# Performance work log

Hardware: AMD Instinct MI355X
Metric: run time of the kernel (lower is better)

The kernel has to match this reference:

```python
import jax, jax.numpy as jnp
import numpy as np
from jax import lax

B, C, HW = 8, 512, 32
NH = 8            # num_heads
NG = 32           # num_groups
HD = C // NH      # head_size = 64
EPS = 1e-6


def group_norm(x, gamma, beta, groups=NG, eps=EPS):
    b, c, h, w = x.shape
    xr = x.reshape(b, groups, c // groups, h, w)
    mu = xr.mean(axis=(2, 3, 4), keepdims=True)
    var = xr.var(axis=(2, 3, 4), keepdims=True)
    xn = ((xr - mu) / jnp.sqrt(var + eps)).reshape(b, c, h, w)
    return xn * gamma[None, :, None, None] + beta[None, :, None, None]


def conv2d(x, w, b):
    y = lax.conv_general_dilated(x, w, (1, 1), 'SAME',
                                 dimension_numbers=('NCHW', 'OIHW', 'NCHW'))
    return y + b[None, :, None, None]


def setup_inputs() -> dict:
    key = jax.random.key(0)
    ks = jax.random.split(key, 24)
    f32 = jnp.float32

    def lin(k, out_d, in_d):
        return (jax.random.normal(k, (out_d, in_d), f32) / np.sqrt(in_d)).astype(f32)

    inp = {
        'hidden_states': jax.random.normal(ks[0], (B, C, HW, HW), f32),
        'pre_g': jnp.ones(C, f32), 'pre_b': jnp.zeros(C, f32),
        'norm_g': jnp.ones(C, f32), 'norm_b': jnp.zeros(C, f32),
        'post_g': jnp.ones(C, f32), 'post_b': jnp.zeros(C, f32),
        'pos_emb': jax.random.normal(ks[1], (1, C, 32, 32), f32) * 0.02,
        'sa_w1': (jax.random.normal(ks[2], (C // 8, C, 1, 1), f32) / np.sqrt(C)),
        'sa_b1': jnp.zeros(C // 8, f32),
        'sa_w2': (jax.random.normal(ks[3], (C // 8, C // 8, 3, 3), f32) / np.sqrt(9 * C // 8)),
        'sa_b2': jnp.zeros(C // 8, f32),
        'sa_w3': (jax.random.normal(ks[4], (1, C // 8, 1, 1), f32) / np.sqrt(C // 8)),
        'sa_b3': jnp.zeros(1, f32),
        'wq': lin(ks[5], C, C), 'wk': lin(ks[6], C, C), 'wv': lin(ks[7], C, C),
        'wq0': lin(ks[8], C // 2, C), 'wk0': lin(ks[9], C // 2, C), 'wv0': lin(ks[10], C // 2, C),
        'wq1': lin(ks[11], C // 2, C), 'wk1': lin(ks[12], C // 2, C), 'wv1': lin(ks[13], C // 2, C),
        'ff_w1': lin(ks[14], C, 2 * C), 'ff_b1': jnp.zeros(C, f32),
        'ff_w2': lin(ks[15], C, C), 'ff_b2': jnp.zeros(C, f32),
        'out_w': lin(ks[16], C, C), 'out_b': jnp.zeros(C, f32),
    }
    return inp


def reference(hidden_states, pre_g, pre_b, norm_g, norm_b, post_g, post_b,
              pos_emb, sa_w1, sa_b1, sa_w2, sa_b2, sa_w3, sa_b3,
              wq, wk, wv, wq0, wk0, wv0, wq1, wk1, wv1,
              ff_w1, ff_b1, ff_w2, ff_b2, out_w, out_b):
    b, c, h, w = hidden_states.shape
    S = h * w
    residual = hidden_states

    hs = group_norm(hidden_states, pre_g, pre_b)
    # H=W=32 matches pos_embedding; bilinear resize to same size is identity
    hs = hs + pos_emb

    # spatial attention gating (conv 1x1 -> SiLU -> conv 3x3 -> SiLU -> conv 1x1 -> sigmoid)
    a = jax.nn.silu(conv2d(hs, sa_w1, sa_b1))
    a = jax.nn.silu(conv2d(a, sa_w2, sa_b2))
    spatial_weights = jax.nn.sigmoid(conv2d(a, sa_w3, sa_b3))
    spatial_enhanced = hs * spatial_weights

    # standard multi-head self-attention over flattened tokens
    sh = group_norm(hs, norm_g, norm_b).reshape(b, c, S).transpose(0, 2, 1)  # (B,S,C)
    ehs = sh  # encoder_hidden_states defaults to standard_hidden

    q = (sh @ wq.T).reshape(b, S, NH, HD)
    k = (ehs @ wk.T).reshape(b, S, NH, HD)
    v = (ehs @ wv.T).reshape(b, S, NH, HD)
    scores = jnp.einsum('bqhd,bkhd->bhqk', q, k) / np.sqrt(HD)
    probs = jax.nn.softmax(scores, axis=-1)
    std_out = jnp.einsum('bhqk,bkhd->bqhd', probs, v).reshape(b, S, c)

    # two multi-scale single-head attention branches (dim C/2 each)
    msh = spatial_enhanced.reshape(b, c, S).transpose(0, 2, 1)  # (B,S,C)
    parts = []
    for wqm, wkm, wvm in ((wq0, wk0, wv0), (wq1, wk1, wv1)):
        qm = msh @ wqm.T          # (B,S,C/2)
        km = ehs @ wkm.T
        vm = ehs @ wvm.T
        sc = jnp.einsum('bqd,bkd->bqk', qm, km) / np.sqrt(c // 2)
        parts.append(jnp.einsum('bqk,bkd->bqd', jax.nn.softmax(sc, axis=-1), vm))
    multi_out = jnp.concatenate(parts, axis=-1)  # (B,S,C)

    combined = jnp.concatenate([std_out, multi_out], axis=-1)  # (B,S,2C)
    fused = jax.nn.silu(combined @ ff_w1.T + ff_b1) @ ff_w2.T + ff_b2  # dropout = eval identity
    final = fused @ out_w.T + out_b
    final = final.transpose(0, 2, 1).reshape(b, c, h, w)
    final = group_norm(final, post_g, post_b)
    return final + residual
```

## Files before the change

### kernel.cpp

```cpp
#include <hip/hip_runtime.h>
#include <hip/hip_bf16.h>
#include <math.h>

typedef __attribute__((ext_vector_type(8))) __bf16 v8bf;
typedef __attribute__((ext_vector_type(4))) float v4f;

__device__ __forceinline__ unsigned short f2bf(float f) {
  union { float f; unsigned int u; } a; a.f = f;
  unsigned int r = a.u + 0x7fffu + ((a.u >> 16) & 1u);
  return (unsigned short)(r >> 16);
}
__device__ __forceinline__ unsigned short f2bf_trunc(float f) {
  union { float f; unsigned int u; } a; a.f = f;
  return (unsigned short)(a.u >> 16);
}
__device__ __forceinline__ float bf2f(unsigned short u) {
  union { unsigned int i; float f; } a; a.i = ((unsigned int)u) << 16; return a.f;
}
__device__ __forceinline__ float sigm(float x) { return 1.0f / (1.0f + __expf(-x)); }

__device__ __forceinline__ void async16(const void* g, void* l) {
  __builtin_amdgcn_global_load_lds(
      (const __attribute__((address_space(1))) unsigned int*)g,
      (__attribute__((address_space(3))) unsigned int*)l, 16, 0, 0);
}

__global__ __launch_bounds__(256) void gn_pre_kernel(
    const float* __restrict__ x, const float* __restrict__ g, const float* __restrict__ be,
    const float* __restrict__ pos, unsigned short* __restrict__ hsb, float* __restrict__ stats) {
  __shared__ float L[16384];
  __shared__ float rs[4], rs2[4], mr[2];
  int b = blockIdx.x >> 5, grp = blockIdx.x & 31;
  const float4* base = (const float4*)(x + ((size_t)b*512 + grp*16)*1024);
  float4* L4 = (float4*)L;
  int w = threadIdx.x >> 6;
  float s = 0.f, s2 = 0.f;
  for (int i = threadIdx.x; i < 4096; i += 256) {
    float4 v = base[i];
    L4[i] = v;
    s += v.x + v.y + v.z + v.w;
    s2 += v.x*v.x + v.y*v.y + v.z*v.z + v.w*v.w;
  }
#pragma unroll
  for (int o = 32; o; o >>= 1) { s += __shfl_xor(s, o); s2 += __shfl_xor(s2, o); }
  if ((threadIdx.x & 63) == 0) { rs[w] = s; rs2[w] = s2; }
  __syncthreads();
  if (threadIdx.x == 0) {
    float ts = rs[0]+rs[1]+rs[2]+rs[3], ts2 = rs2[0]+rs2[1]+rs2[2]+rs2[3];
    float mu = ts * (1.0f/16384.0f);
    float var = ts2 * (1.0f/16384.0f) - mu*mu;
    mr[0] = mu; mr[1] = rsqrtf(var + 1e-6f);
  }
  __syncthreads();
  float mu = mr[0], rstd = mr[1];
  const float4* pb = (const float4*)(pos + (size_t)grp*16*1024);
  float ns = 0.f, ns2 = 0.f;
  for (int i = threadIdx.x; i < 4096; i += 256) {
    float4 v = L4[i], p = pb[i];
    int c = grp*16 + (i >> 8);
    float gg = g[c], bb = be[c];
    float4 o;
    o.x = (v.x - mu)*rstd*gg + bb + p.x;
    o.y = (v.y - mu)*rstd*gg + bb + p.y;
    o.z = (v.z - mu)*rstd*gg + bb + p.z;
    o.w = (v.w - mu)*rstd*gg + bb + p.w;
    L4[i] = o;
    ns += o.x + o.y + o.z + o.w;
    ns2 += o.x*o.x + o.y*o.y + o.z*o.z + o.w*o.w;
  }
#pragma unroll
  for (int o = 32; o; o >>= 1) { ns += __shfl_xor(ns, o); ns2 += __shfl_xor(ns2, o); }
  if ((threadIdx.x & 63) == 0) { rs[w] = ns; rs2[w] = ns2; }
  __syncthreads();
  if (threadIdx.x == 0) {
    float ts = rs[0]+rs[1]+rs[2]+rs[3], ts2 = rs2[0]+rs2[1]+rs2[2]+rs2[3];
    float nmu = ts * (1.0f/16384.0f);
    float nvar = ts2 * (1.0f/16384.0f) - nmu*nmu;
    stats[(b*32+grp)*2] = nmu; stats[(b*32+grp)*2+1] = rsqrtf(nvar + 1e-6f);
  }
#pragma unroll
  for (int j = 0; j < 4; ++j) {
    int sI = threadIdx.x + j*256;
    unsigned int wd[8];
#pragma unroll
    for (int c = 0; c < 8; ++c) {
      unsigned int lo = f2bf(L[(2*c)*1024 + sI]);
      unsigned int hi = f2bf(L[(2*c+1)*1024 + sI]);
      wd[c] = lo | (hi << 16);
    }
    size_t oo = (size_t)(b*1024 + sI)*512 + grp*16;
    *(uint4*)(hsb + oo)     = make_uint4(wd[0], wd[1], wd[2], wd[3]);
    *(uint4*)(hsb + oo + 8) = make_uint4(wd[4], wd[5], wd[6], wd[7]);
  }
}

__global__ __launch_bounds__(256) void im2col_kernel(
    const unsigned short* __restrict__ a1, unsigned short* __restrict__ im2) {
  int row0 = blockIdx.x * 8;
#pragma unroll
  for (int it = 0; it < 3; ++it) {
    int cc = it*256 + threadIdx.x;
    if (cc >= 576) break;
    int rl = cc / 72, rr = cc - rl*72;
    int tap = rr >> 3, ch8 = rr & 7;
    int row = row0 + rl;
    int bb = row >> 10, s = row & 1023;
    int y = s >> 5, xx0 = s & 31;
    int yy = y + tap/3 - 1, xx = xx0 + tap%3 - 1;
    ushort4 v0 = make_ushort4(0,0,0,0), v1 = make_ushort4(0,0,0,0);
    if ((unsigned)yy < 32u && (unsigned)xx < 32u) {
      const unsigned short* src = a1 + ((size_t)(bb*1024 + yy*32 + xx))*64 + ch8*8;
      v0 = *(const ushort4*)src; v1 = *(const ushort4*)(src + 4);
    }
    unsigned short* dst = im2 + (size_t)row*576 + tap*64 + ch8*8;
    *(ushort4*)dst = v0; *(ushort4*)(dst + 4) = v1;
  }
}

__global__ __launch_bounds__(256) void gate_norm_kernel(
    const unsigned short* __restrict__ hsb, const unsigned short* __restrict__ a2,
    const float* __restrict__ w3, const float* __restrict__ b3,
    const float* __restrict__ stats, const float* __restrict__ g,
    const float* __restrict__ be,
    unsigned short* __restrict__ sh, unsigned short* __restrict__ msh) {
  int b = blockIdx.y;
  int s = blockIdx.x * 4 + (threadIdx.x >> 6);
  int oct = threadIdx.x & 63;
  int c0 = oct * 8;
  int grp = c0 >> 4;
  float part = bf2f(a2[((size_t)(b*1024) + s)*64 + oct]) * w3[oct];
#pragma unroll
  for (int o = 32; o; o >>= 1) part += __shfl_xor(part, o);
  float wgt = sigm(part + b3[0]);
  float mu = stats[(b*32 + grp)*2], rstd = stats[(b*32 + grp)*2 + 1];
  size_t o = (size_t)(b*1024 + s)*512 + c0;
  ushort4 u0 = *(const ushort4*)(hsb + o), u1 = *(const ushort4*)(hsb + o + 4);
  unsigned short uu[8] = {u0.x,u0.y,u0.z,u0.w,u1.x,u1.y,u1.z,u1.w};
  unsigned short so[8], mo[8];
#pragma unroll
  for (int j = 0; j < 8; ++j) {
    float v = bf2f(uu[j]);
    so[j] = f2bf((v - mu)*rstd*g[c0+j] + be[c0+j]);
    mo[j] = f2bf(v * wgt);
  }
  *(ushort4*)(sh + o)     = make_ushort4(so[0], so[1], so[2], so[3]);
  *(ushort4*)(sh + o + 4) = make_ushort4(so[4], so[5], so[6], so[7]);
  *(ushort4*)(msh + o)     = make_ushort4(mo[0], mo[1], mo[2], mo[3]);
  *(ushort4*)(msh + o + 4) = make_ushort4(mo[4], mo[5], mo[6], mo[7]);
}

struct WCvt { const float* src; int dstOff; int n; float scale; };
struct WCvtArgs { WCvt w[15]; };
__global__ __launch_bounds__(256) void wconvert_kernel(WCvtArgs a, unsigned short* __restrict__ dst) {
  WCvt e = a.w[blockIdx.y];
  int i = blockIdx.x * 256 + threadIdx.x;
  if (i >= e.n) return;
  if (blockIdx.y == 13) {
    int oc = i / 576, r = i - oc*576;
    int tap = r >> 6, ic = r & 63;
    dst[e.dstOff + i] = f2bf(e.src[(oc*64 + ic)*9 + tap]);
  } else if (blockIdx.y == 14) {
    dst[e.dstOff + i] = f2bf(e.src[(i & 511)*512 + (i >> 9)]);
  } else {
    dst[e.dstOff + i] = f2bf(e.src[i] * e.scale);
  }
}

__global__ __launch_bounds__(256) void bias_fold_kernel(
    const float* __restrict__ ow, const float* __restrict__ b2,
    const float* __restrict__ ob, float* __restrict__ bc) {
  int n = blockIdx.x * 256 + threadIdx.x;
  float s = ob[n];
  const float* r = ow + (size_t)n * 512;
#pragma unroll 8
  for (int j = 0; j < 512; ++j) s += r[j] * b2[j];
  bc[n] = s;
}

__global__ __launch_bounds__(256) void transpose2_kernel(
    const unsigned short* __restrict__ qkvm,
    unsigned short* __restrict__ vtb, unsigned short* __restrict__ vmt) {
  __shared__ unsigned short t[64][65];
  int s0 = blockIdx.x * 64, c0 = blockIdx.y * 64;
  int z = blockIdx.z, b = z & 7;
  const unsigned short* in = qkvm + (z >= 8 ? 2048 : 1024);
  unsigned short* out = (z >= 8) ? vmt : vtb;
  int tx = threadIdx.x & 63, ty = threadIdx.x >> 6;
#pragma unroll
  for (int i = 0; i < 16; ++i) {
    int s = ty + i*4;
    t[s][tx] = in[((size_t)(b*1024 + s0 + s))*2560 + c0 + tx];
  }
  __syncthreads();
#pragma unroll
  for (int i = 0; i < 16; ++i) {
    int c = ty + i*4;
    out[((size_t)b*512 + c0 + c)*1024 + s0 + tx] = t[tx][c];
  }
}

struct GemmDesc {
  const unsigned short* A; const unsigned short* B; void* out; const float* bias;
  int M, N, K, lda, ldb, ldo, epi;
  long long Ay, Az, By, Bz, Oy, Oz;
};

template<int BM, int BN>
__global__ __launch_bounds__(256) void gemm_tile_kernel(GemmDesc d) {
  constexpr int WGM = (BN >= 128) ? 2 : 4;
  constexpr int WGN = 4 / WGM;
  constexpr int MT = BM / (16 * WGM);
  constexpr int NT = BN / (16 * WGN);
  constexpr int AIT = (BM * 8) / 256;
  constexpr int BIT = (BN * 8) / 256;
  __shared__ __align__(16) unsigned short As[BM * 64];
  __shared__ __align__(16) unsigned short Bs[BN * 64];

  int ntx = d.N / BN, mtx = d.M / BM;
  int bmt, bnt;
  if ((mtx & 7) == 0) {
    int xcd = blockIdx.x & 7, j = blockIdx.x >> 3;
    int mpx = mtx >> 3;
    bmt = xcd * mpx + (j % mpx);
    bnt = j / mpx;
  } else {
    bmt = blockIdx.x / ntx; bnt = blockIdx.x % ntx;
  }
  int bm0 = bmt * BM, bn0 = bnt * BN;
  const unsigned short* A = d.A + (long long)blockIdx.y * d.Ay
      + (long long)blockIdx.z * d.Az + (size_t)bm0 * d.lda;
  const unsigned short* B = d.B + (long long)blockIdx.y * d.By
      + (long long)blockIdx.z * d.Bz + (size_t)bn0 * d.ldb;
  int tid = threadIdx.x, lane = tid & 63, w = tid >> 6;
  int wm = (WGN == 2) ? (w >> 1) : w;
  int wn = (WGN == 2) ? (w & 1) : 0;
  int ln = lane & 15, qd = lane >> 4;

  v4f acc[MT][NT];
#pragma unroll
  for (int i = 0; i < MT; ++i)
#pragma unroll
    for (int j = 0; j < NT; ++j) acc[i][j] = (v4f){0.f, 0.f, 0.f, 0.f};

  int nks = d.K >> 6;
  for (int ks = 0; ks < nks; ++ks) {
    int kof = ks * 64;
#pragma unroll
    for (int it = 0; it < AIT; ++it) {
      int c = it * 256 + tid;
      int row = c >> 3, ch = c & 7;
      async16(A + (size_t)row * d.lda + ((ch ^ (row & 7)) << 3) + kof, As + c * 8);
    }
#pragma unroll
    for (int it = 0; it < BIT; ++it) {
      int c = it * 256 + tid;
      int row = c >> 3, ch = c & 7;
      async16(B + (size_t)row * d.ldb + ((ch ^ (row & 7)) << 3) + kof, Bs + c * 8);
    }
    __syncthreads();
#pragma unroll
    for (int k2 = 0; k2 < 2; ++k2) {
      v8bf af[MT], bfr[NT];
#pragma unroll
      for (int i = 0; i < MT; ++i) {
        int row = wm * MT * 16 + i * 16 + ln;
        af[i] = *(const v8bf*)(As + row * 64 + (((k2*4 + qd) ^ (ln & 7)) << 3));
      }
#pragma unroll
      for (int j = 0; j < NT; ++j) {
        int row = wn * NT * 16 + j * 16 + ln;
        bfr[j] = *(const v8bf*)(Bs + row * 64 + (((k2*4 + qd) ^ (ln & 7)) << 3));
      }
#pragma unroll
      for (int i = 0; i < MT; ++i)
#pragma unroll
        for (int j = 0; j < NT; ++j)
          acc[i][j] = __builtin_amdgcn_mfma_f32_16x16x32_bf16(af[i], bfr[j], acc[i][j], 0, 0, 0);
    }
    __syncthreads();
  }

  size_t obase = (size_t)((long long)blockIdx.y * d.Oy + (long long)blockIdx.z * d.Oz);
#pragma unroll
  for (int i = 0; i < MT; ++i) {
#pragma unroll
    for (int j = 0; j < NT; ++j) {
      int col = bn0 + wn * NT * 16 + j * 16 + ln;
      float bia = d.bias ? d.bias[col] : 0.0f;
#pragma unroll
      for (int r = 0; r < 4; ++r) {
        int row = bm0 + wm * MT * 16 + i * 16 + qd * 4 + r;
        float v = acc[i][j][r] + bia;
        if (d.epi == 2) v = v * sigm(v);
        size_t oi = obase + (size_t)row * d.ldo + col;
        if (d.epi == 0) ((float*)d.out)[oi] = v;
        else ((unsigned short*)d.out)[oi] = f2bf(v);
      }
    }
  }
}

__global__ __launch_bounds__(512) void flash_attn_kernel(
    const unsigned short* __restrict__ QKVM, const unsigned short* __restrict__ VTB,
    unsigned short* __restrict__ out) {
  __shared__ __align__(16) unsigned short Ks[128*64];
  __shared__ __align__(16) unsigned short Vts[64*128];
  __shared__ __align__(16) unsigned short Pw[8][32*128];
  int h = blockIdx.x, b = blockIdx.y, qt = blockIdx.z;
  int tid = threadIdx.x, lane = tid & 63, w = tid >> 6;
  int ln = lane & 15, qd = lane >> 4;

  const unsigned short* Qbase = QKVM + ((size_t)(b*1024 + qt*256 + w*32))*2560 + h*64;
  v8bf aq[2][2];
#pragma unroll
  for (int i = 0; i < 2; ++i)
#pragma unroll
    for (int s = 0; s < 2; ++s)
      aq[i][s] = *(const v8bf*)(Qbase + (size_t)(i*16 + ln)*2560 + s*32 + qd*8);

  v4f o_acc[2][4];
  float l_part[2][4];
#pragma unroll
  for (int i = 0; i < 2; ++i) {
#pragma unroll
    for (int dn = 0; dn < 4; ++dn) o_acc[i][dn] = (v4f){0.f,0.f,0.f,0.f};
#pragma unroll
    for (int r = 0; r < 4; ++r) l_part[i][r] = 0.f;
  }

  const unsigned short* Kg = QKVM + 512 + (size_t)(b*1024)*2560 + h*64;
  const unsigned short* Vg = VTB + ((size_t)(b*512) + h*64)*1024;

  for (int kt = 0; kt < 8; ++kt) {
#pragma unroll
    for (int it = 0; it < 2; ++it) {
      int c = it*512 + tid;
      async16(Kg + (size_t)(kt*128 + (c >> 3))*2560 + (((c & 7) ^ ((c >> 3) & 7)) << 3),
              Ks + c*8);
    }
#pragma unroll
    for (int it = 0; it < 2; ++it) {
      int c = it*512 + tid;
      async16(Vg + (size_t)(c >> 4)*1024 + kt*128 + ((((c & 15) ^ ((c >> 4) & 7))) << 3),
              Vts + c*8);
    }
    __syncthreads();

    v4f sc[2][8];
#pragma unroll
    for (int i = 0; i < 2; ++i)
#pragma unroll
      for (int n = 0; n < 8; ++n) sc[i][n] = (v4f){0.f,0.f,0.f,0.f};
#pragma unroll
    for (int n = 0; n < 8; ++n)
#pragma unroll
      for (int s = 0; s < 2; ++s) {
        v8bf kb = *(const v8bf*)(Ks + (n*16 + ln)*64 + (((s*4 + qd) ^ (ln & 7)) << 3));
#pragma unroll
        for (int i = 0; i < 2; ++i)
          sc[i][n] = __builtin_amdgcn_mfma_f32_16x16x32_bf16(aq[i][s], kb, sc[i][n], 0, 0, 0);
      }
#pragma unroll
    for (int i = 0; i < 2; ++i)
#pragma unroll
      for (int r = 0; r < 4; ++r) {
        int row7 = (qd*4 + r) & 7;
        float acc_l = 0.f;
#pragma unroll
        for (int n = 0; n < 8; ++n) {
          float p = exp2f(sc[i][n][r]);
          acc_l += p;
          Pw[w][(i*16 + qd*4 + r)*128 + (((n*2 + (ln >> 3)) ^ row7) << 3) + (ln & 7)] = f2bf_trunc(p);
        }
        l_part[i][r] += acc_l;
      }
    v8bf pf[2][4];
#pragma unroll
    for (int i = 0; i < 2; ++i)
#pragma unroll
      for (int ks2 = 0; ks2 < 4; ++ks2)
        pf[i][ks2] = *(const v8bf*)(&Pw[w][(i*16 + ln)*128 + (((ks2*4 + qd) ^ (ln & 7)) << 3)]);
#pragma unroll
    for (int dn = 0; dn < 4; ++dn)
#pragma unroll
      for (int ks2 = 0; ks2 < 4; ++ks2) {
        v8bf vf = *(const v8bf*)(Vts + (dn*16 + ln)*128 + (((ks2*4 + qd) ^ (ln & 7)) << 3));
#pragma unroll
        for (int i = 0; i < 2; ++i)
          o_acc[i][dn] = __builtin_amdgcn_mfma_f32_16x16x32_bf16(pf[i][ks2], vf, o_acc[i][dn], 0, 0, 0);
      }
    __syncthreads();
  }

  unsigned short* ob = out + ((size_t)(b*1024 + qt*256 + w*32))*1024 + h*64;
#pragma unroll
  for (int i = 0; i < 2; ++i)
#pragma unroll
    for (int r = 0; r < 4; ++r) {
      float l = l_part[i][r];
      l += __shfl_xor(l, 1); l += __shfl_xor(l, 2);
      l += __shfl_xor(l, 4); l += __shfl_xor(l, 8);
      float rinv = 1.0f / l;
#pragma unroll
      for (int dn = 0; dn < 4; ++dn)
        ob[(size_t)(i*16 + qd*4 + r)*1024 + dn*16 + ln] = f2bf(o_acc[i][dn][r] * rinv);
    }
}

__global__ __launch_bounds__(256) void flash_branch_kernel(
    const unsigned short* __restrict__ QKVM, const unsigned short* __restrict__ QM,
    const unsigned short* __restrict__ VMT, float* __restrict__ OP, float* __restrict__ LP) {
  __shared__ __align__(16) unsigned short Ks[64*256];
  __shared__ __align__(16) unsigned short Vts[256*64];
  __shared__ __align__(16) unsigned short Pw[4][32*64];
  int bb = blockIdx.x, b = bb >> 1, br = bb & 1;
  int kh = blockIdx.y, qt = blockIdx.z;
  int tid = threadIdx.x, lane = tid & 63, w = tid >> 6;
  int ln = lane & 15, qd = lane >> 4;

  const unsigned short* Qb = QM + ((size_t)(b*1024 + qt*128 + w*32))*512 + br*256;
  v8bf aq[2][8];
#pragma unroll
  for (int i = 0; i < 2; ++i)
#pragma unroll
    for (int s = 0; s < 8; ++s)
      aq[i][s] = *(const v8bf*)(Qb + (size_t)(i*16 + ln)*512 + s*32 + qd*8);

  v4f o_acc[2][16];
  float l_part[2][4];
#pragma unroll
  for (int i = 0; i < 2; ++i) {
#pragma unroll
    for (int dn = 0; dn < 16; ++dn) o_acc[i][dn] = (v4f){0.f,0.f,0.f,0.f};
#pragma unroll
    for (int r = 0; r < 4; ++r) l_part[i][r] = 0.f;
  }

  const unsigned short* Kg = QKVM + 1536 + br*256 + (size_t)(b*1024)*2560;
  const unsigned short* Vg = VMT + ((size_t)(b*512) + br*256)*1024;

  for (int kt = kh*8; kt < kh*8 + 8; ++kt) {
#pragma unroll
    for (int it = 0; it < 8; ++it) {
      int c = it*256 + tid;
      int row = c >> 5, ch = c & 31;
      async16(Kg + (size_t)(kt*64 + row)*2560 + ((ch ^ (row & 7)) << 3), Ks + c*8);
    }
#pragma unroll
    for (int it = 0; it < 8; ++it) {
      int c = it*256 + tid;
      int row = c >> 3, ch = c & 7;
      async16(Vg + (size_t)row*1024 + kt*64 + ((ch ^ (row & 7)) << 3), Vts + c*8);
    }
    __syncthreads();

    v4f sc[2][4];
#pragma unroll
    for (int i = 0; i < 2; ++i)
#pragma unroll
      for (int n = 0; n < 4; ++n) sc[i][n] = (v4f){0.f,0.f,0.f,0.f};
#pragma unroll
    for (int n = 0; n < 4; ++n)
#pragma unroll
      for (int s = 0; s < 8; ++s) {
        v8bf kb = *(const v8bf*)(Ks + (n*16 + ln)*256 + (((s*4 + qd) ^ (ln & 7)) << 3));
#pragma unroll
        for (int i = 0; i < 2; ++i)
          sc[i][n] = __builtin_amdgcn_mfma_f32_16x16x32_bf16(aq[i][s], kb, sc[i][n], 0, 0, 0);
      }
#pragma unroll
    for (int i = 0; i < 2; ++i)
#pragma unroll
      for (int r = 0; r < 4; ++r) {
        int row7 = (qd*4 + r) & 7;
        float acc_l = 0.f;
#pragma unroll
        for (int n = 0; n < 4; ++n) {
          float p = exp2f(sc[i][n][r]);
          acc_l += p;
          Pw[w][(i*16 + qd*4 + r)*64 + (((n*2 + (ln >> 3)) ^ row7) << 3) + (ln & 7)] = f2bf_trunc(p);
        }
        l_part[i][r] += acc_l;
      }
    v8bf pf[2][2];
#pragma unroll
    for (int i = 0; i < 2; ++i)
#pragma unroll
      for (int ks2 = 0; ks2 < 2; ++ks2)
        pf[i][ks2] = *(const v8bf*)(&Pw[w][(i*16 + ln)*64 + (((ks2*4 + qd) ^ (ln & 7)) << 3)]);
#pragma unroll
    for (int dn = 0; dn < 16; ++dn)
#pragma unroll
      for (int ks2 = 0; ks2 < 2; ++ks2) {
        v8bf vf = *(const v8bf*)(Vts + (dn*16 + ln)*64 + (((ks2*4 + qd) ^ (ln & 7)) << 3));
#pragma unroll
        for (int i = 0; i < 2; ++i)
          o_acc[i][dn] = __builtin_amdgcn_mfma_f32_16x16x32_bf16(pf[i][ks2], vf, o_acc[i][dn], 0, 0, 0);
      }
    __syncthreads();
  }

  int slot = ((bb*8 + qt)*2 + kh);
  float* Ob = OP + (size_t)slot*32768;
  float* Lb = LP + (size_t)slot*128;
#pragma unroll
  for (int i = 0; i < 2; ++i)
#pragma unroll
    for (int r = 0; r < 4; ++r) {
      int row = w*32 + i*16 + qd*4 + r;
      float l = l_part[i][r];
      l += __shfl_xor(l, 1); l += __shfl_xor(l, 2);
      l += __shfl_xor(l, 4); l += __shfl_xor(l, 8);
      if (ln == 0) Lb[row] = l;
#pragma unroll
      for (int dn = 0; dn < 16; ++dn)
        Ob[(size_t)row*256 + dn*16 + ln] = o_acc[i][dn][r];
    }
}

__global__ __launch_bounds__(256) void branch_combine_kernel(
    const float* __restrict__ OP, const float* __restrict__ LP,
    unsigned short* __restrict__ out) {
  int bb = blockIdx.x, qt = blockIdx.y;
  int b = bb >> 1, br = bb & 1;
  int slot0 = (bb*8 + qt)*2, slot1 = slot0 + 1;
  int row = threadIdx.x >> 1, cseg = (threadIdx.x & 1) * 128;
  float l = LP[(size_t)slot0*128 + row] + LP[(size_t)slot1*128 + row];
  float rinv = 1.0f / l;
  const float4* o0 = (const float4*)(OP + (size_t)slot0*32768 + (size_t)row*256 + cseg);
  const float4* o1 = (const float4*)(OP + (size_t)slot1*32768 + (size_t)row*256 + cseg);
  unsigned short* ob = out + ((size_t)(b*1024 + qt*128 + row))*1024 + 512 + br*256 + cseg;
#pragma unroll
  for (int i = 0; i < 32; ++i) {
    float4 a = o0[i], c = o1[i];
    ob[i*4+0] = f2bf((a.x + c.x) * rinv);
    ob[i*4+1] = f2bf((a.y + c.y) * rinv);
    ob[i*4+2] = f2bf((a.z + c.z) * rinv);
    ob[i*4+3] = f2bf((a.w + c.w) * rinv);
  }
}

__global__ __launch_bounds__(256) void gn_stats_bf16_kernel(
    const unsigned short* __restrict__ t, float* __restrict__ stats) {
  int b = blockIdx.x >> 5, grp = blockIdx.x & 31;
  float s = 0.f, s2 = 0.f;
#pragma unroll
  for (int j = 0; j < 4; ++j) {
    int sI = threadIdx.x + j*256;
    const unsigned short* p = t + ((size_t)(b*1024 + sI))*512 + grp*16;
    uint4 a = *(const uint4*)p, c2 = *(const uint4*)(p + 8);
    unsigned int ww[8] = {a.x,a.y,a.z,a.w,c2.x,c2.y,c2.z,c2.w};
#pragma unroll
    for (int k = 0; k < 8; ++k) {
      float lo = bf2f((unsigned short)(ww[k] & 0xffff));
      float hi = bf2f((unsigned short)(ww[k] >> 16));
      s += lo + hi; s2 += lo*lo + hi*hi;
    }
  }
#pragma unroll
  for (int o = 32; o; o >>= 1) { s += __shfl_xor(s, o); s2 += __shfl_xor(s2, o); }
  __shared__ float rs[4], rs2[4];
  int w = threadIdx.x >> 6;
  if ((threadIdx.x & 63) == 0) { rs[w] = s; rs2[w] = s2; }
  __syncthreads();
  if (threadIdx.x == 0) {
    float ts = rs[0]+rs[1]+rs[2]+rs[3], ts2 = rs2[0]+rs2[1]+rs2[2]+rs2[3];
    float mu = ts * (1.0f/16384.0f);
    float var = ts2 * (1.0f/16384.0f) - mu*mu;
    stats[(b*32+grp)*2] = mu; stats[(b*32+grp)*2+1] = rsqrtf(var + 1e-6f);
  }
}

__global__ __launch_bounds__(256) void final_out_kernel(
    const unsigned short* __restrict__ fin, const float* __restrict__ stats,
    const float* __restrict__ g, const float* __restrict__ be,
    const float* __restrict__ x, float* __restrict__ out) {
  __shared__ float t[64][65];
  int s0 = blockIdx.x * 64, c0 = blockIdx.y * 64, b = blockIdx.z;
  int tx = threadIdx.x & 63, ty = threadIdx.x >> 6;
#pragma unroll
  for (int i = 0; i < 16; ++i) {
    int s = ty + i*4;
    t[s][tx] = bf2f(fin[((size_t)(b*1024 + s0 + s))*512 + c0 + tx]);
  }
  __syncthreads();
#pragma unroll
  for (int i = 0; i < 16; ++i) {
    int c = ty + i*4;
    int cc = c0 + c, grp = cc >> 4;
    float mu = stats[(b*32+grp)*2], rstd = stats[(b*32+grp)*2+1];
    float gg = g[cc], bb = be[cc];
    size_t oi = ((size_t)(b*512 + cc))*1024 + s0 + tx;
    out[oi] = (t[tx][c] - mu)*rstd*gg + bb + x[oi];
  }
}

static void launch_gemm128(hipStream_t st, const unsigned short* A, const unsigned short* B,
                           void* out, const float* bias,
                           int M, int N, int K, int lda, int ldb, int ldo, int epi,
                           long long Ay, long long Az, long long By, long long Bz,
                           long long Oy, long long Oz, int gy, int gz) {
  GemmDesc d{A, B, out, bias, M, N, K, lda, ldb, ldo, epi, Ay, Az, By, Bz, Oy, Oz};
  gemm_tile_kernel<128,128><<<dim3((M/128)*(N/128), gy, gz), dim3(256), 0, st>>>(d);
}
static void launch_gemm64(hipStream_t st, const unsigned short* A, const unsigned short* B,
                          void* out, const float* bias,
                          int M, int N, int K, int lda, int ldb, int ldo, int epi) {
  GemmDesc d{A, B, out, bias, M, N, K, lda, ldb, ldo, epi, 0,0,0,0,0,0};
  gemm_tile_kernel<128,64><<<dim3((M/128)*(N/64), 1, 1), dim3(256), 0, st>>>(d);
}

extern "C" void kernel_launch(void* const* d_in, const int* in_sizes, int n_in,
                              void* d_out, int out_size, void* d_ws, size_t ws_size,
                              hipStream_t stream) {
  const float* x      = (const float*)d_in[0];
  const float* pre_g  = (const float*)d_in[1];
  const float* pre_b  = (const float*)d_in[2];
  const float* norm_g = (const float*)d_in[3];
  const float* norm_b = (const float*)d_in[4];
  const float* post_g = (const float*)d_in[5];
  const float* post_b = (const float*)d_in[6];
  const float* pos    = (const float*)d_in[7];
  const float* sa_b1  = (const float*)d_in[9];
  const float* sa_b2  = (const float*)d_in[11];
  const float* sa_w3  = (const float*)d_in[12];
  const float* sa_b3  = (const float*)d_in[13];
  const float* ff_b1  = (const float*)d_in[24];
  const float* ff_b2  = (const float*)d_in[26];
  const float* out_w  = (const float*)d_in[27];
  const float* out_b  = (const float*)d_in[28];
  float* outp = (float*)d_out;

  char* ws = (char*)d_ws;
  size_t off = 0;
  auto alloc = [&](size_t bytes) -> void* {
    void* p = ws + off; off += (bytes + 255) & ~(size_t)255; return p;
  };
  float* STATS = (float*)alloc(4096);
  float* BC    = (float*)alloc(2048);
  unsigned short* HSB  = (unsigned short*)alloc(8388608);
  unsigned short* A1   = (unsigned short*)alloc(1048576);
  unsigned short* IM2  = (unsigned short*)alloc(9437184);
  unsigned short* A2   = (unsigned short*)alloc(1048576);
  unsigned short* SHB  = (unsigned short*)alloc(8388608);
  unsigned short* MSHB = (unsigned short*)alloc(8388608);
  unsigned short* WBF  = (unsigned short*)alloc(6291456);
  unsigned short* WCOMB= (unsigned short*)alloc(524288);
  unsigned short* QKVM = (unsigned short*)alloc(41943040);
  unsigned short* QM   = (unsigned short*)alloc(8388608);
  unsigned short* VTB  = (unsigned short*)alloc(8388608);
  unsigned short* VMT  = (unsigned short*)alloc(8388608);
  unsigned short* COMB = (unsigned short*)alloc(16777216);
  unsigned short* FFMID= (unsigned short*)alloc(8388608);
  unsigned short* FINALB=(unsigned short*)alloc(8388608);
  float* OP    = (float*)alloc(33554432);
  float* LP    = (float*)alloc(131072);

  const int OQKVM=0, OQM=1310720, OFF1=1572864, OFF2T=2097152,
            OOW=2359296, OW1=2621440, OW2R=2654208;

  gn_pre_kernel<<<dim3(256), dim3(256), 0, stream>>>(x, pre_g, pre_b, pos, HSB, STATS);
  {
    WCvtArgs a;
    const float LG2E = 1.4426950408889634f;
    const int   srcIdx[15] = {14,15,16, 18,21,19,22, 17,20, 23,27, 8, 0, 10, 25};
    const int   dofs[15]   = {0, 262144, 524288,
                              786432, 917504, 1048576, 1179648,
                              OQM, OQM+131072,
                              OFF1, OOW, OW1, 0, OW2R, OFF2T};
    const int   ns[15]     = {262144,262144,262144, 131072,131072,131072,131072,
                              131072,131072, 524288,262144, 32768, 0, 36864, 262144};
    const float sc[15]     = {0.125f*LG2E,1.f,1.f, 1.f,1.f,1.f,1.f,
                              0.0625f*LG2E,0.0625f*LG2E, 1.f,1.f, 1.f, 0.f, 1.f, 1.f};
    for (int i = 0; i < 15; ++i) { a.w[i].src = (const float*)d_in[srcIdx[i]]; a.w[i].dstOff = dofs[i]; a.w[i].n = ns[i]; a.w[i].scale = sc[i]; }
    wconvert_kernel<<<dim3(2048, 15), dim3(256), 0, stream>>>(a, WBF);
  }
  {
    GemmDesc d{WBF+OOW, WBF+OFF2T, WCOMB, nullptr, 512, 512, 512, 512, 512, 512, 1, 0,0,0,0,0,0};
    gemm_tile_kernel<128,128><<<dim3(16, 1, 1), dim3(256), 0, stream>>>(d);
  }
  bias_fold_kernel<<<dim3(2), dim3(256), 0, stream>>>(out_w, ff_b2, out_b, BC);
  launch_gemm64(stream, HSB, WBF+OW1,  A1, sa_b1, 8192, 64, 512, 512, 512, 64, 2);
  im2col_kernel<<<dim3(1024), dim3(256), 0, stream>>>(A1, IM2);
  launch_gemm64(stream, IM2, WBF+OW2R, A2, sa_b2, 8192, 64, 576, 576, 576, 64, 2);
  gate_norm_kernel<<<dim3(256, 8), dim3(256), 0, stream>>>(HSB, A2, sa_w3, sa_b3, STATS, norm_g, norm_b, SHB, MSHB);

  launch_gemm128(stream, SHB,  WBF+OQKVM, QKVM, nullptr, 8192, 2560, 512, 512, 512, 2560, 1, 0,0,0,0,0,0, 1,1);
  launch_gemm64(stream, MSHB, WBF+OQM,   QM,   nullptr, 8192, 512,  512, 512, 512, 512,  1);

  transpose2_kernel<<<dim3(16, 8, 16), dim3(256), 0, stream>>>(QKVM, VTB, VMT);

  flash_attn_kernel<<<dim3(8, 8, 4), dim3(512), 0, stream>>>(QKVM, VTB, COMB);

  flash_branch_kernel<<<dim3(16, 2, 8), dim3(256), 0, stream>>>(QKVM, QM, VMT, OP, LP);
  branch_combine_kernel<<<dim3(16, 8), dim3(256), 0, stream>>>(OP, LP, COMB);

  launch_gemm64(stream, COMB,  WBF+OFF1, FFMID,  ff_b1, 8192, 512, 1024, 1024, 1024, 512, 2);
  launch_gemm64(stream, FFMID, WCOMB,    FINALB, BC,    8192, 512, 512,  512,  512,  512, 1);

  gn_stats_bf16_kernel<<<dim3(256), dim3(256), 0, stream>>>(FINALB, STATS);
  final_out_kernel<<<dim3(16, 8, 8), dim3(256), 0, stream>>>(FINALB, STATS, post_g, post_b, x, outp);

  (void)in_sizes; (void)n_in; (void)out_size; (void)ws_size;
}
```

Measured before the change: 400.5 us.

## Split branch attention keys four ways with smaller tiles and bf16 partials

The multi-scale branch flash kernel now splits the 1024 keys into four chunks instead of two, using 32-key tiles, which doubles the grid to 256 blocks and shrinks shared memory per block. Partial outputs are written as bf16 instead of fp32, and the combine kernel sums four partials using vectorized 16-byte loads and stores. The goal is better occupancy and CU fill, plus less partial-buffer traffic. In exchange there are more, smaller iterations, an extra rounding of the partials to bf16, and the V tile no longer uses the XOR swizzle, so LDS bank conflicts may appear.

```diff
diff --git a/kernel.cpp b/kernel.cpp
--- a/kernel.cpp
+++ b/kernel.cpp
@@ -409,10 +409,11 @@
 
 __global__ __launch_bounds__(256) void flash_branch_kernel(
     const unsigned short* __restrict__ QKVM, const unsigned short* __restrict__ QM,
-    const unsigned short* __restrict__ VMT, float* __restrict__ OP, float* __restrict__ LP) {
-  __shared__ __align__(16) unsigned short Ks[64*256];
-  __shared__ __align__(16) unsigned short Vts[256*64];
-  __shared__ __align__(16) unsigned short Pw[4][32*64];
+    const unsigned short* __restrict__ VMT, unsigned short* __restrict__ OPH,
+    float* __restrict__ LP) {
+  __shared__ __align__(16) unsigned short Ks[32*256];
+  __shared__ __align__(16) unsigned short Vts[256*32];
+  __shared__ __align__(16) unsigned short Pw[4][32*32];
   int bb = blockIdx.x, b = bb >> 1, br = bb & 1;
   int kh = blockIdx.y, qt = blockIdx.z;
   int tid = threadIdx.x, lane = tid & 63, w = tid >> 6;
@@ -441,26 +442,26 @@
 
   for (int kt = kh*8; kt < kh*8 + 8; ++kt) {
 #pragma unroll
-    for (int it = 0; it < 8; ++it) {
+    for (int it = 0; it < 4; ++it) {
       int c = it*256 + tid;
       int row = c >> 5, ch = c & 31;
-      async16(Kg + (size_t)(kt*64 + row)*2560 + ((ch ^ (row & 7)) << 3), Ks + c*8);
-    }
-#pragma unroll
-    for (int it = 0; it < 8; ++it) {
+      async16(Kg + (size_t)(kt*32 + row)*2560 + ((ch ^ (row & 7)) << 3), Ks + c*8);
+    }
+#pragma unroll
+    for (int it = 0; it < 4; ++it) {
       int c = it*256 + tid;
-      int row = c >> 3, ch = c & 7;
-      async16(Vg + (size_t)row*1024 + kt*64 + ((ch ^ (row & 7)) << 3), Vts + c*8);
+      int row = c >> 2, ch = c & 3;
+      async16(Vg + (size_t)row*1024 + kt*32 + (ch << 3), Vts + c*8);
     }
     __syncthreads();
 
-    v4f sc[2][4];
+    v4f sc[2][2];
 #pragma unroll
     for (int i = 0; i < 2; ++i)
 #pragma unroll
-      for (int n = 0; n < 4; ++n) sc[i][n] = (v4f){0.f,0.f,0.f,0.f};
-#pragma unroll
-    for (int n = 0; n < 4; ++n)
+      for (int n = 0; n < 2; ++n) sc[i][n] = (v4f){0.f,0.f,0.f,0.f};
+#pragma unroll
+    for (int n = 0; n < 2; ++n)
 #pragma unroll
       for (int s = 0; s < 8; ++s) {
         v8bf kb = *(const v8bf*)(Ks + (n*16 + ln)*256 + (((s*4 + qd) ^ (ln & 7)) << 3));
@@ -472,36 +473,31 @@
     for (int i = 0; i < 2; ++i)
 #pragma unroll
       for (int r = 0; r < 4; ++r) {
-        int row7 = (qd*4 + r) & 7;
         float acc_l = 0.f;
 #pragma unroll
-        for (int n = 0; n < 4; ++n) {
+        for (int n = 0; n < 2; ++n) {
           float p = exp2f(sc[i][n][r]);
           acc_l += p;
-          Pw[w][(i*16 + qd*4 + r)*64 + (((n*2 + (ln >> 3)) ^ row7) << 3) + (ln & 7)] = f2bf_trunc(p);
+          Pw[w][(i*16 + qd*4 + r)*32 + (((n*2 + (ln >> 3)) ^ r) << 3) + (ln & 7)] = f2bf_trunc(p);
         }
         l_part[i][r] += acc_l;
       }
-    v8bf pf[2][2];
+    v8bf pf[2];
 #pragma unroll
     for (int i = 0; i < 2; ++i)
-#pragma unroll
-      for (int ks2 = 0; ks2 < 2; ++ks2)
-        pf[i][ks2] = *(const v8bf*)(&Pw[w][(i*16 + ln)*64 + (((ks2*4 + qd) ^ (ln & 7)) << 3)]);
-#pragma unroll
-    for (int dn = 0; dn < 16; ++dn)
-#pragma unroll
-      for (int ks2 = 0; ks2 < 2; ++ks2) {
-        v8bf vf = *(const v8bf*)(Vts + (dn*16 + ln)*64 + (((ks2*4 + qd) ^ (ln & 7)) << 3));
-#pragma unroll
-        for (int i = 0; i < 2; ++i)
-          o_acc[i][dn] = __builtin_amdgcn_mfma_f32_16x16x32_bf16(pf[i][ks2], vf, o_acc[i][dn], 0, 0, 0);
-      }
+      pf[i] = *(const v8bf*)(&Pw[w][(i*16 + ln)*32 + ((qd ^ (ln & 3)) << 3)]);
+#pragma unroll
+    for (int dn = 0; dn < 16; ++dn) {
+      v8bf vf = *(const v8bf*)(Vts + (dn*16 + ln)*32 + (qd << 3));
+#pragma unroll
+      for (int i = 0; i < 2; ++i)
+        o_acc[i][dn] = __builtin_amdgcn_mfma_f32_16x16x32_bf16(pf[i], vf, o_acc[i][dn], 0, 0, 0);
+    }
     __syncthreads();
   }
 
-  int slot = ((bb*8 + qt)*2 + kh);
-  float* Ob = OP + (size_t)slot*32768;
+  int slot = (bb*8 + qt)*4 + kh;
+  unsigned short* Ob = OPH + (size_t)slot*32768;
   float* Lb = LP + (size_t)slot*128;
 #pragma unroll
   for (int i = 0; i < 2; ++i)
@@ -514,29 +510,43 @@
       if (ln == 0) Lb[row] = l;
 #pragma unroll
       for (int dn = 0; dn < 16; ++dn)
-        Ob[(size_t)row*256 + dn*16 + ln] = o_acc[i][dn][r];
+        Ob[(size_t)row*256 + dn*16 + ln] = f2bf(o_acc[i][dn][r]);
     }
 }
 
 __global__ __launch_bounds__(256) void branch_combine_kernel(
-    const float* __restrict__ OP, const float* __restrict__ LP,
+    const unsigned short* __restrict__ OPH, const float* __restrict__ LP,
     unsigned short* __restrict__ out) {
   int bb = blockIdx.x, qt = blockIdx.y;
   int b = bb >> 1, br = bb & 1;
-  int slot0 = (bb*8 + qt)*2, slot1 = slot0 + 1;
+  int s0 = (bb*8 + qt)*4;
   int row = threadIdx.x >> 1, cseg = (threadIdx.x & 1) * 128;
-  float l = LP[(size_t)slot0*128 + row] + LP[(size_t)slot1*128 + row];
+  float l = LP[(size_t)s0*128 + row] + LP[(size_t)(s0+1)*128 + row]
+          + LP[(size_t)(s0+2)*128 + row] + LP[(size_t)(s0+3)*128 + row];
   float rinv = 1.0f / l;
-  const float4* o0 = (const float4*)(OP + (size_t)slot0*32768 + (size_t)row*256 + cseg);
-  const float4* o1 = (const float4*)(OP + (size_t)slot1*32768 + (size_t)row*256 + cseg);
   unsigned short* ob = out + ((size_t)(b*1024 + qt*128 + row))*1024 + 512 + br*256 + cseg;
 #pragma unroll
-  for (int i = 0; i < 32; ++i) {
-    float4 a = o0[i], c = o1[i];
-    ob[i*4+0] = f2bf((a.x + c.x) * rinv);
-    ob[i*4+1] = f2bf((a.y + c.y) * rinv);
-    ob[i*4+2] = f2bf((a.z + c.z) * rinv);
-    ob[i*4+3] = f2bf((a.w + c.w) * rinv);
+  for (int j = 0; j < 16; ++j) {
+    float acc[8] = {0,0,0,0,0,0,0,0};
+#pragma unroll
+    for (int k = 0; k < 4; ++k) {
+      const unsigned short* p = OPH + (size_t)(s0+k)*32768 + (size_t)row*256 + cseg + j*8;
+      uint4 u = *(const uint4*)p;
+      unsigned int ww[4] = {u.x, u.y, u.z, u.w};
+#pragma unroll
+      for (int e = 0; e < 4; ++e) {
+        acc[e*2]   += bf2f((unsigned short)(ww[e] & 0xffff));
+        acc[e*2+1] += bf2f((unsigned short)(ww[e] >> 16));
+      }
+    }
+    unsigned int wd[4];
+#pragma unroll
+    for (int e = 0; e < 4; ++e) {
+      unsigned int lo = f2bf(acc[e*2] * rinv);
+      unsigned int hi = f2bf(acc[e*2+1] * rinv);
+      wd[e] = lo | (hi << 16);
+    }
+    *(uint4*)(ob + j*8) = make_uint4(wd[0], wd[1], wd[2], wd[3]);
   }
 }
 
@@ -653,8 +663,8 @@
   unsigned short* COMB = (unsigned short*)alloc(16777216);
   unsigned short* FFMID= (unsigned short*)alloc(8388608);
   unsigned short* FINALB=(unsigned short*)alloc(8388608);
-  float* OP    = (float*)alloc(33554432);
-  float* LP    = (float*)alloc(131072);
+  unsigned short* OPH  = (unsigned short*)alloc(33554432);
+  float* LP    = (float*)alloc(262144);
 
   const int OQKVM=0, OQM=1310720, OFF1=1572864, OFF2T=2097152,
             OOW=2359296, OW1=2621440, OW2R=2654208;
@@ -692,8 +702,8 @@
 
   flash_attn_kernel<<<dim3(8, 8, 4), dim3(512), 0, stream>>>(QKVM, VTB, COMB);
 
-  flash_branch_kernel<<<dim3(16, 2, 8), dim3(256), 0, stream>>>(QKVM, QM, VMT, OP, LP);
-  branch_combine_kernel<<<dim3(16, 8), dim3(256), 0, stream>>>(OP, LP, COMB);
+  flash_branch_kernel<<<dim3(16, 4, 8), dim3(256), 0, stream>>>(QKVM, QM, VMT, OPH, LP);
+  branch_combine_kernel<<<dim3(16, 8), dim3(256), 0, stream>>>(OPH, LP, COMB);
 
   launch_gemm64(stream, COMB,  WBF+OFF1, FFMID,  ff_b1, 8192, 512, 1024, 1024, 1024, 512, 2);
   launch_gemm64(stream, FFMID, WCOMB,    FINALB, BC,    8192, 512, 512,  512,  512,  512, 1);
```

Result: slower. 413.5 us (+3.3%).
